# Optimization experiments

Measured on AMD Instinct MI355X. Metric: run time of the kernel, lower is better.

## Reference

```python
import jax, jax.numpy as jnp
import numpy as np

B, S, V = 256, 512, 50000
E, PD, PS = 256, 32, 121
FN, TAG = 230, 53
FEAT = E + 2 * PD  # 320
NEG = -1e30


def setup_inputs() -> dict:
    key = jax.random.key(0)
    ks = jax.random.split(key, 12)
    sentence = jax.random.randint(ks[0], (B, S), 0, V)
    # relative-position ids; 60 marks the entity token, keep background < 60
    pos1 = jax.random.randint(ks[1], (B, S), 0, 60)
    pos2 = jax.random.randint(ks[2], (B, S), 0, 60)
    e1 = jax.random.randint(ks[3], (B,), 1, S // 3)            # entity1 in first third
    e2 = jax.random.randint(ks[4], (B,), S // 3 + 1, 2 * S // 3)  # entity2 in second third
    rows = jnp.arange(B)
    pos1 = pos1.at[rows, e1].set(60)
    pos2 = pos2.at[rows, e2].set(60)
    word_emb = 0.02 * jax.random.normal(ks[5], (V, E), dtype=jnp.float32)
    pos1_emb = 0.02 * jax.random.normal(ks[6], (PS, PD), dtype=jnp.float32)
    pos2_emb = 0.02 * jax.random.normal(ks[7], (PS, PD), dtype=jnp.float32)
    rel_emb = 0.02 * jax.random.normal(ks[8], (TAG, FN), dtype=jnp.float32)
    conv_w = 0.05 * jax.random.normal(ks[9], (3, FEAT, FN), dtype=jnp.float32)  # HIO
    conv_b = jnp.zeros((FN,), dtype=jnp.float32)
    att_weight = jax.random.normal(ks[10], (B, 1, FN), dtype=jnp.float32)
    relation_bias = jax.random.normal(ks[11], (B, TAG, 1), dtype=jnp.float32)
    return {"sentence": sentence, "pos1": pos1, "pos2": pos2,
            "word_emb": word_emb, "pos1_emb": pos1_emb, "pos2_emb": pos2_emb,
            "rel_emb": rel_emb, "conv_w": conv_w, "conv_b": conv_b,
            "att_weight": att_weight, "relation_bias": relation_bias}


def reference(sentence, pos1, pos2, word_emb, pos1_emb, pos2_emb,
              rel_emb, conv_w, conv_b, att_weight, relation_bias):
    # embedding concat: [B, S, FEAT]
    embeds = jnp.concatenate(
        [word_emb[sentence], pos1_emb[pos1], pos2_emb[pos2]], axis=2)
    # Conv2d(1, FN, (3, FEAT), padding=(1, 0)) == 1D conv over seq, SAME-ish pad 1
    cnn = jax.lax.conv_general_dilated(
        embeds, conv_w, window_strides=(1,), padding=[(1, 1)],
        dimension_numbers=("NHC", "HIO", "NHC"))  # [B, S, FN]
    cnn = jax.nn.relu(cnn + conv_b)

    # vectorized entity segment boundaries (replaces the Python batch loop)
    idx = jnp.arange(S)
    mk1 = pos1 == 60
    mk2 = pos2 == 60
    p1min = jnp.min(jnp.where(mk1, idx, S), axis=1)
    p1max = jnp.max(jnp.where(mk1, idx, -1), axis=1)
    p2min = jnp.min(jnp.where(mk2, idx, S), axis=1)
    p2max = jnp.max(jnp.where(mk2, idx, -1), axis=1)
    first = p1min < p2min
    m1 = jnp.where(first, p1min, p2min)
    m2 = jnp.where(first, p1max, p2max)
    m3 = jnp.where(first, p2min, p1min)
    m4 = jnp.where(first, p2max, p1max)

    t = idx[None, :]  # [1, S]
    mask_a = t < jnp.maximum(m1, 1)[:, None]
    mask_b = (t >= m2[:, None]) & (t < jnp.maximum(m3, m2 + 1)[:, None])
    mask_c = t >= m4[:, None]

    def seg_max(mask):
        return jnp.max(jnp.where(mask[:, :, None], cnn, NEG), axis=1)  # [B, FN]

    pcnn = jnp.stack([seg_max(mask_a), seg_max(mask_b), seg_max(mask_c)], axis=2)  # [B, FN, 3]

    # attention over the 3 pooled segments
    M = jnp.tanh(pcnn)
    scores = jnp.einsum("bof,bft->bot", att_weight, M)      # [B, 1, 3]
    a = jax.nn.softmax(scores, axis=2)
    att = jnp.einsum("bft,bot->bfo", pcnn, a)               # [B, FN, 1]
    att_out = jnp.tanh(att)

    wei = jnp.einsum("tf,bfo->bto", rel_emb, att_out)       # [B, TAG, 1]
    res = jax.nn.softmax(wei + relation_bias, axis=1)
    return res.reshape(B, -1)
```

## Files before the change

kernel.cpp:

```cpp
#include <hip/hip_runtime.h>
#include <hip/hip_bf16.h>
#include <math.h>

constexpr int B    = 256;
constexpr int S    = 512;
constexpr int E    = 256;
constexpr int PD   = 32;
constexpr int FEAT = 320;
constexpr int FN   = 230;
constexpr int FNP  = 256;
constexpr int TAG  = 53;
constexpr int K    = 960;
constexpr int BM   = 128;
constexpr int KS   = 32;
constexpr int NG   = 10;
constexpr int LDA  = 36;
constexpr int LDB  = 36;

typedef short  bf16x8 __attribute__((ext_vector_type(8)));
typedef float  f32x4  __attribute__((ext_vector_type(4)));

__device__ __forceinline__ unsigned f2bf(float x) {
    union { float f; unsigned u; } v; v.f = x;
    unsigned r = v.u + 0x7FFF + ((v.u >> 16) & 1);
    return r >> 16;
}
__device__ __forceinline__ unsigned pack2(float a, float b) {
    return f2bf(a) | (f2bf(b) << 16);
}

__global__ __launch_bounds__(256) void wt_prep_kernel(
    const float* __restrict__ conv_w, unsigned short* __restrict__ wt)
{
    __shared__ float tile[32][33];
    const int tx = threadIdx.x & 31;
    const int ty = threadIdx.x >> 5;
    const int k0 = blockIdx.x * 32;
    const int n0 = blockIdx.y * 32;
#pragma unroll
    for (int i = 0; i < 4; ++i) {
        int k = k0 + ty + i * 8;
        int n = n0 + tx;
        tile[ty + i * 8][tx] = (n < FN) ? conv_w[(size_t)k * FN + n] : 0.0f;
    }
    __syncthreads();
#pragma unroll
    for (int i = 0; i < 4; ++i) {
        int n = n0 + ty + i * 8;
        int k = k0 + tx;
        wt[(size_t)n * K + k] = (unsigned short)f2bf(tile[tx][ty + i * 8]);
    }
}

__global__ __launch_bounds__(256) void bounds_kernel(
    const int* __restrict__ pos1, const int* __restrict__ pos2,
    int* __restrict__ segb, unsigned* __restrict__ pcnn)
{
    const int b = blockIdx.x;
    const int tid = threadIdx.x;
    __shared__ int r[4];
    if (tid == 0) { r[0] = S; r[1] = -1; r[2] = S; r[3] = -1; }
    __syncthreads();
    for (int s = tid; s < S; s += 256) {
        if (pos1[b * S + s] == 60) { atomicMin(&r[0], s); atomicMax(&r[1], s); }
        if (pos2[b * S + s] == 60) { atomicMin(&r[2], s); atomicMax(&r[3], s); }
    }
    __syncthreads();
    if (tid == 0) {
        int p1min = r[0], p1max = r[1], p2min = r[2], p2max = r[3];
        bool first = p1min < p2min;
        int m1 = first ? p1min : p2min;
        int m2 = first ? p1max : p2max;
        int m3 = first ? p2min : p1min;
        int m4 = first ? p2max : p1max;
        int4 o;
        o.x = max(m1, 1);
        o.y = m2;
        o.z = max(m3, m2 + 1);
        o.w = m4;
        *(int4*)(segb + b * 4) = o;
    }
    unsigned* pc = pcnn + (size_t)b * 3 * FNP;
    for (int i = tid; i < 3 * FNP; i += 256) pc[i] = 0u;
}

__global__ __launch_bounds__(512, 4) void conv_mfma_kernel(
    const int* __restrict__ sentence, const int* __restrict__ pos1,
    const int* __restrict__ pos2,
    const float* __restrict__ word_emb, const float* __restrict__ pos1_emb,
    const float* __restrict__ pos2_emb,
    const unsigned short* __restrict__ wt, const float* __restrict__ conv_b,
    const int* __restrict__ segb, unsigned* __restrict__ pcnn)
{
    __shared__ __align__(16) unsigned short ldsA[(BM + 2) * LDA];
    __shared__ __align__(16) unsigned short ldsB[FNP * LDB];
    __shared__ unsigned maxbuf[3 * FNP];

    const int tid  = threadIdx.x;
    const int b    = blockIdx.y;
    const int s0   = blockIdx.x * BM;
    const int lane = tid & 63;
    const int wid  = tid >> 6;
    const int wm   = wid >> 2;
    const int wn   = wid & 3;
    const int lrow = lane & 15;
    const int lgrp = lane >> 4;

    for (int i = tid; i < 3 * FNP; i += 512) maxbuf[i] = 0u;

    const int* sent_b = sentence + b * S;
    const int* p1_b   = pos1 + b * S;
    const int* p2_b   = pos2 + b * S;

    f32x4 acc[4][4];
#pragma unroll
    for (int i = 0; i < 4; ++i)
#pragma unroll
        for (int j = 0; j < 4; ++j) acc[i][j] = (f32x4){0.f, 0.f, 0.f, 0.f};

    for (int g = 0; g < NG; ++g) {
        const int fb = g * KS;

        __syncthreads();

        {
            int c = tid;
#pragma unroll
            for (int rep = 0; rep < 2; ++rep, c += 512) {
                if (c < (BM + 2) * 4) {
                    int r = c >> 2, q = c & 3;
                    int s = s0 - 1 + r;
                    int feat = fb + q * 8;
                    float4 v0 = make_float4(0.f, 0.f, 0.f, 0.f);
                    float4 v1 = v0;
                    if (s >= 0 && s < S) {
                        const float* p;
                        if (feat < E)            p = word_emb + (size_t)sent_b[s] * E + feat;
                        else if (feat < E + PD)  p = pos1_emb + p1_b[s] * PD + (feat - E);
                        else                     p = pos2_emb + p2_b[s] * PD + (feat - E - PD);
                        v0 = *(const float4*)p;
                        v1 = *(const float4*)(p + 4);
                    }
                    uint4 pk;
                    pk.x = pack2(v0.x, v0.y);
                    pk.y = pack2(v0.z, v0.w);
                    pk.z = pack2(v1.x, v1.y);
                    pk.w = pack2(v1.z, v1.w);
                    *(uint4*)&ldsA[r * LDA + q * 8] = pk;
                }
            }
        }
        {
            int c = tid;
#pragma unroll
            for (int rep = 0; rep < 2; ++rep, c += 512) {
                int n = c >> 2, q = c & 3;
                uint4 v = *(const uint4*)(wt + (size_t)n * K + fb + q * 8);
                *(uint4*)&ldsB[n * LDB + q * 8] = v;
            }
        }
        __syncthreads();

#pragma unroll
        for (int w = 0; w < 3; ++w) {
            bf16x8 af[4], bfr[4];
#pragma unroll
            for (int mi = 0; mi < 4; ++mi) {
                int r = wm * 64 + mi * 16 + lrow + w;
                af[mi] = *(const bf16x8*)&ldsA[r * LDA + lgrp * 8];
            }
#pragma unroll
            for (int ni = 0; ni < 4; ++ni) {
                if (wn * 64 + ni * 16 < FN) {
                    int n = wn * 64 + ni * 16 + lrow;
                    bfr[ni] = *(const bf16x8*)&ldsB[n * LDB + lgrp * 8];
                }
            }
#pragma unroll
            for (int mi = 0; mi < 4; ++mi)
#pragma unroll
                for (int ni = 0; ni < 4; ++ni)
                    if (wn * 64 + ni * 16 < FN)
                        acc[mi][ni] = __builtin_amdgcn_mfma_f32_16x16x32_bf16(
                            af[mi], bfr[ni], acc[mi][ni], 0, 0, 0);

            if (w < 2) {
                __syncthreads();
                int c = tid;
#pragma unroll
                for (int rep = 0; rep < 2; ++rep, c += 512) {
                    int n = c >> 2, q = c & 3;
                    uint4 v = *(const uint4*)(wt + (size_t)n * K
                                              + (w + 1) * FEAT + fb + q * 8);
                    *(uint4*)&ldsB[n * LDB + q * 8] = v;
                }
                __syncthreads();
            }
        }
    }

    const int4 sb = *(const int4*)(segb + b * 4);
    float biasv[4];
#pragma unroll
    for (int ni = 0; ni < 4; ++ni) {
        int f = wn * 64 + ni * 16 + lrow;
        biasv[ni] = (f < FN) ? conv_b[f] : 0.0f;
    }
#pragma unroll
    for (int mi = 0; mi < 4; ++mi) {
#pragma unroll
        for (int r = 0; r < 4; ++r) {
            int s = s0 + wm * 64 + mi * 16 + lgrp * 4 + r;
            int mask = 0;
            if (s < sb.x) mask |= 1;
            if (s >= sb.y && s < sb.z) mask |= 2;
            if (s >= sb.w) mask |= 4;
            if (!mask) continue;
#pragma unroll
            for (int ni = 0; ni < 4; ++ni) {
                int f = wn * 64 + ni * 16 + lrow;
                if (f >= FN) continue;
                float v = fmaxf(acc[mi][ni][r] + biasv[ni], 0.0f);
                unsigned uv = __float_as_uint(v);
                if (mask & 1) atomicMax(&maxbuf[f], uv);
                if (mask & 2) atomicMax(&maxbuf[FNP + f], uv);
                if (mask & 4) atomicMax(&maxbuf[2 * FNP + f], uv);
            }
        }
    }
    __syncthreads();
    unsigned* pc = pcnn + (size_t)b * 3 * FNP;
    for (int i = tid; i < 3 * FNP; i += 512) {
        unsigned m = maxbuf[i];
        if (((i & (FNP - 1)) < FN) && m) atomicMax(pc + i, m);
    }
}

__global__ __launch_bounds__(256) void finale_kernel(
    const float* __restrict__ pcnn, const float* __restrict__ att_weight,
    const float* __restrict__ rel_emb, const float* __restrict__ rel_bias,
    float* __restrict__ out)
{
    const int b = blockIdx.x;
    const int tid = threadIdx.x;
    __shared__ float red[12];
    __shared__ float satt[FN];
    __shared__ float wtag[56];

    const float* pc = pcnn + (size_t)b * 3 * FNP;
    float p0 = 0.f, p1 = 0.f, p2 = 0.f, aw = 0.f;
    if (tid < FN) {
        p0 = pc[tid];
        p1 = pc[FNP + tid];
        p2 = pc[2 * FNP + tid];
        aw = att_weight[b * FN + tid];
    }
    const int wid = tid >> 6;
#pragma unroll
    for (int t = 0; t < 3; ++t) {
        float pt = (t == 0) ? p0 : (t == 1) ? p1 : p2;
        float r = (tid < FN) ? aw * tanhf(pt) : 0.0f;
#pragma unroll
        for (int o = 32; o; o >>= 1) r += __shfl_xor(r, o);
        if ((tid & 63) == 0) red[t * 4 + wid] = r;
    }
    __syncthreads();
    float sc0 = red[0] + red[1] + red[2] + red[3];
    float sc1 = red[4] + red[5] + red[6] + red[7];
    float sc2 = red[8] + red[9] + red[10] + red[11];
    float m3s = fmaxf(sc0, fmaxf(sc1, sc2));
    float e0 = expf(sc0 - m3s), e1 = expf(sc1 - m3s), e2 = expf(sc2 - m3s);
    float inv = 1.0f / (e0 + e1 + e2);
    float a0 = e0 * inv, a1 = e1 * inv, a2 = e2 * inv;
    if (tid < FN) satt[tid] = tanhf(p0 * a0 + p1 * a1 + p2 * a2);
    __syncthreads();

    const int t = tid >> 2;
    const int part = tid & 3;
    if (t < TAG) {
        float s = 0.0f;
        for (int f = part; f < FN; f += 4) s += rel_emb[t * FN + f] * satt[f];
        s += __shfl_xor(s, 1);
        s += __shfl_xor(s, 2);
        if (part == 0) wtag[t] = s + rel_bias[b * TAG + t];
    }
    __syncthreads();

    if (tid < 64) {
        float v = (tid < TAG) ? wtag[tid] : -1e30f;
        float mx = v;
#pragma unroll
        for (int o = 32; o; o >>= 1) mx = fmaxf(mx, __shfl_xor(mx, o));
        float e = (tid < TAG) ? expf(v - mx) : 0.0f;
        float sum = e;
#pragma unroll
        for (int o = 32; o; o >>= 1) sum += __shfl_xor(sum, o);
        if (tid < TAG) out[b * TAG + tid] = e / sum;
    }
}

extern "C" void kernel_launch(void* const* d_in, const int* in_sizes, int n_in,
                              void* d_out, int out_size, void* d_ws, size_t ws_size,
                              hipStream_t stream)
{
    const int*   sentence  = (const int*)d_in[0];
    const int*   pos1      = (const int*)d_in[1];
    const int*   pos2      = (const int*)d_in[2];
    const float* word_emb  = (const float*)d_in[3];
    const float* pos1_emb  = (const float*)d_in[4];
    const float* pos2_emb  = (const float*)d_in[5];
    const float* rel_emb   = (const float*)d_in[6];
    const float* conv_w    = (const float*)d_in[7];
    const float* conv_b    = (const float*)d_in[8];
    const float* att_w     = (const float*)d_in[9];
    const float* rel_bias  = (const float*)d_in[10];
    float* out = (float*)d_out;

    int*            segb = (int*)d_ws;
    unsigned*       pcnn = (unsigned*)((char*)d_ws + 4096);
    unsigned short* wt   = (unsigned short*)((char*)d_ws + 4096 + 786432);

    wt_prep_kernel<<<dim3(K / 32, FNP / 32), 256, 0, stream>>>(conv_w, wt);
    bounds_kernel<<<B, 256, 0, stream>>>(pos1, pos2, segb, pcnn);
    conv_mfma_kernel<<<dim3(S / BM, B), 512, 0, stream>>>(
        sentence, pos1, pos2, word_emb, pos1_emb, pos2_emb,
        wt, conv_b, segb, pcnn);
    finale_kernel<<<B, 256, 0, stream>>>(
        (const float*)pcnn, att_w, rel_emb, rel_bias, out);
}
```

Before: 224.5 us.

## Restructure conv GEMM loads: direct-to-LDS weights, register-prefetched embeddings, merged prep kernel

Merges the weight-transpose and segment-bounds kernels into one launch, and reorders the weight layout so that each K-group's three conv taps are contiguous. The conv kernel now loads all three taps of B per group with global_load_lds straight into LDS, which removes the per-tap barriers and reloads. The embedding gather for the next group is prefetched into registers while the MFMAs run, and MFMA priority is raised via setprio. This cuts synchronisation and global-load latency per iteration, at the cost of a larger LDS footprint (about 49KB for B) that may lower occupancy.

```diff
diff --git a/kernel.cpp b/kernel.cpp
--- a/kernel.cpp
+++ b/kernel.cpp
@@ -1,21 +1,15 @@
 #include <hip/hip_runtime.h>
-#include <hip/hip_bf16.h>
 #include <math.h>
 
 constexpr int B    = 256;
 constexpr int S    = 512;
 constexpr int E    = 256;
 constexpr int PD   = 32;
-constexpr int FEAT = 320;
 constexpr int FN   = 230;
 constexpr int FNP  = 256;
 constexpr int TAG  = 53;
-constexpr int K    = 960;
 constexpr int BM   = 128;
-constexpr int KS   = 32;
 constexpr int NG   = 10;
-constexpr int LDA  = 36;
-constexpr int LDB  = 36;
 
 typedef short  bf16x8 __attribute__((ext_vector_type(8)));
 typedef float  f32x4  __attribute__((ext_vector_type(4)));
@@ -29,59 +23,64 @@
     return f2bf(a) | (f2bf(b) << 16);
 }
 
-__global__ __launch_bounds__(256) void wt_prep_kernel(
-    const float* __restrict__ conv_w, unsigned short* __restrict__ wt)
-{
-    __shared__ float tile[32][33];
-    const int tx = threadIdx.x & 31;
-    const int ty = threadIdx.x >> 5;
-    const int k0 = blockIdx.x * 32;
-    const int n0 = blockIdx.y * 32;
-#pragma unroll
-    for (int i = 0; i < 4; ++i) {
-        int k = k0 + ty + i * 8;
-        int n = n0 + tx;
-        tile[ty + i * 8][tx] = (n < FN) ? conv_w[(size_t)k * FN + n] : 0.0f;
-    }
-    __syncthreads();
-#pragma unroll
-    for (int i = 0; i < 4; ++i) {
-        int n = n0 + ty + i * 8;
-        int k = k0 + tx;
-        wt[(size_t)n * K + k] = (unsigned short)f2bf(tile[tx][ty + i * 8]);
-    }
-}
-
-__global__ __launch_bounds__(256) void bounds_kernel(
-    const int* __restrict__ pos1, const int* __restrict__ pos2,
+__device__ __forceinline__ void gl_lds16(const void* g, void* l) {
+    __builtin_amdgcn_global_load_lds(
+        (const __attribute__((address_space(1))) unsigned int*)g,
+        (__attribute__((address_space(3))) unsigned int*)l, 16, 0, 0);
+}
+
+__global__ __launch_bounds__(256) void prep_kernel(
+    const float* __restrict__ conv_w, const int* __restrict__ pos1,
+    const int* __restrict__ pos2, unsigned short* __restrict__ wt2,
     int* __restrict__ segb, unsigned* __restrict__ pcnn)
 {
-    const int b = blockIdx.x;
+    const int bid = blockIdx.x;
     const int tid = threadIdx.x;
-    __shared__ int r[4];
-    if (tid == 0) { r[0] = S; r[1] = -1; r[2] = S; r[3] = -1; }
-    __syncthreads();
-    for (int s = tid; s < S; s += 256) {
-        if (pos1[b * S + s] == 60) { atomicMin(&r[0], s); atomicMax(&r[1], s); }
-        if (pos2[b * S + s] == 60) { atomicMin(&r[2], s); atomicMax(&r[3], s); }
-    }
-    __syncthreads();
-    if (tid == 0) {
-        int p1min = r[0], p1max = r[1], p2min = r[2], p2max = r[3];
-        bool first = p1min < p2min;
-        int m1 = first ? p1min : p2min;
-        int m2 = first ? p1max : p2max;
-        int m3 = first ? p2min : p1min;
-        int m4 = first ? p2max : p1max;
-        int4 o;
-        o.x = max(m1, 1);
-        o.y = m2;
-        o.z = max(m3, m2 + 1);
-        o.w = m4;
-        *(int4*)(segb + b * 4) = o;
-    }
-    unsigned* pc = pcnn + (size_t)b * 3 * FNP;
-    for (int i = tid; i < 3 * FNP; i += 256) pc[i] = 0u;
+    if (bid < 240) {
+        __shared__ float tile[32][33];
+        const int kb = bid % 30, nb = bid / 30;
+        const int k0 = kb * 32, n0 = nb * 32;
+        const int tx = tid & 31, ty = tid >> 5;
+#pragma unroll
+        for (int i = 0; i < 4; ++i) {
+            int k = k0 + ty + i * 8, n = n0 + tx;
+            tile[ty + i * 8][tx] = (n < FN) ? conv_w[(size_t)k * FN + n] : 0.0f;
+        }
+        __syncthreads();
+        const int g = (k0 >> 5) % 10, w = k0 / 320;
+#pragma unroll
+        for (int i = 0; i < 4; ++i) {
+            int n = n0 + ty + i * 8;
+            wt2[(size_t)n * 960 + g * 96 + w * 32 + tx] =
+                (unsigned short)f2bf(tile[tx][ty + i * 8]);
+        }
+    } else {
+        const int b = bid - 240;
+        __shared__ int r[4];
+        if (tid == 0) { r[0] = S; r[1] = -1; r[2] = S; r[3] = -1; }
+        __syncthreads();
+        for (int s = tid; s < S; s += 256) {
+            if (pos1[b * S + s] == 60) { atomicMin(&r[0], s); atomicMax(&r[1], s); }
+            if (pos2[b * S + s] == 60) { atomicMin(&r[2], s); atomicMax(&r[3], s); }
+        }
+        __syncthreads();
+        if (tid == 0) {
+            int p1min = r[0], p1max = r[1], p2min = r[2], p2max = r[3];
+            bool first = p1min < p2min;
+            int m1 = first ? p1min : p2min;
+            int m2 = first ? p1max : p2max;
+            int m3 = first ? p2min : p1min;
+            int m4 = first ? p2max : p1max;
+            int4 o;
+            o.x = max(m1, 1);
+            o.y = m2;
+            o.z = max(m3, m2 + 1);
+            o.w = m4;
+            *(int4*)(segb + b * 4) = o;
+        }
+        unsigned* pc = pcnn + (size_t)b * 3 * FNP;
+        for (int i = tid; i < 3 * FNP; i += 256) pc[i] = 0u;
+    }
 }
 
 __global__ __launch_bounds__(512, 4) void conv_mfma_kernel(
@@ -89,11 +88,11 @@
     const int* __restrict__ pos2,
     const float* __restrict__ word_emb, const float* __restrict__ pos1_emb,
     const float* __restrict__ pos2_emb,
-    const unsigned short* __restrict__ wt, const float* __restrict__ conv_b,
+    const unsigned short* __restrict__ wt2, const float* __restrict__ conv_b,
     const int* __restrict__ segb, unsigned* __restrict__ pcnn)
 {
-    __shared__ __align__(16) unsigned short ldsA[(BM + 2) * LDA];
-    __shared__ __align__(16) unsigned short ldsB[FNP * LDB];
+    __shared__ __align__(16) unsigned short ldsB[12 * 256 * 8];
+    __shared__ __align__(16) unsigned short ldsA[528 * 8];
     __shared__ unsigned maxbuf[3 * FNP];
 
     const int tid  = threadIdx.x;
@@ -108,9 +107,23 @@
 
     for (int i = tid; i < 3 * FNP; i += 512) maxbuf[i] = 0u;
 
-    const int* sent_b = sentence + b * S;
-    const int* p1_b   = pos1 + b * S;
-    const int* p2_b   = pos2 + b * S;
+    const int q0 = (tid >= 396) ? 3 : (tid >= 264) ? 2 : (tid >= 132) ? 1 : 0;
+    const int r0 = tid - q0 * 132;
+    const int sA0 = s0 - 1 + r0;
+    const bool v0 = (unsigned)sA0 < (unsigned)S;
+    const int sid0 = v0 ? sentence[b * S + sA0] : 0;
+    const int p10  = v0 ? pos1[b * S + sA0] : 0;
+    const int p20  = v0 ? pos2[b * S + sA0] : 0;
+    const int r1   = 116 + tid;
+    const int sA1  = s0 - 1 + r1;
+    const bool v1  = (tid < 16) && ((unsigned)sA1 < (unsigned)S);
+    const int sid1 = v1 ? sentence[b * S + sA1] : 0;
+    const int p11  = v1 ? pos1[b * S + sA1] : 0;
+    const int p21  = v1 ? pos2[b * S + sA1] : 0;
+
+    const size_t bnoff = (size_t)(tid & 255) * 1920;
+    const int    bc0   = tid >> 8;
+    const char*  wt2c  = (const char*)wt2;
 
     f32x4 acc[4][4];
 #pragma unroll
@@ -118,64 +131,67 @@
 #pragma unroll
         for (int j = 0; j < 4; ++j) acc[i][j] = (f32x4){0.f, 0.f, 0.f, 0.f};
 
+    auto srcA = [&](int g, int sid, int p1v, int p2v, int qq) -> const float* {
+        if (g < 8)  return word_emb + (size_t)sid * E + g * 32 + qq * 8;
+        if (g == 8) return pos1_emb + p1v * PD + qq * 8;
+        return pos2_emb + p2v * PD + qq * 8;
+    };
+
+    float4 am0, am1, ae0, ae1;
+    {
+        const float* p = srcA(0, sid0, p10, p20, q0);
+        am0 = *(const float4*)p; am1 = *(const float4*)(p + 4);
+        if (tid < 16) {
+            const float* pe = srcA(0, sid1, p11, p21, 3);
+            ae0 = *(const float4*)pe; ae1 = *(const float4*)(pe + 4);
+        }
+    }
+
     for (int g = 0; g < NG; ++g) {
-        const int fb = g * KS;
-
-        __syncthreads();
-
+        __builtin_amdgcn_s_barrier();
+#pragma unroll
+        for (int rep = 0; rep < 6; ++rep) {
+            const void* src = wt2c + bnoff + (size_t)(g * 12 + 2 * rep + bc0) * 16;
+            void* dst = (char*)ldsB + (rep * 512 + wid * 64) * 16;
+            gl_lds16(src, dst);
+        }
         {
-            int c = tid;
-#pragma unroll
-            for (int rep = 0; rep < 2; ++rep, c += 512) {
-                if (c < (BM + 2) * 4) {
-                    int r = c >> 2, q = c & 3;
-                    int s = s0 - 1 + r;
-                    int feat = fb + q * 8;
-                    float4 v0 = make_float4(0.f, 0.f, 0.f, 0.f);
-                    float4 v1 = v0;
-                    if (s >= 0 && s < S) {
-                        const float* p;
-                        if (feat < E)            p = word_emb + (size_t)sent_b[s] * E + feat;
-                        else if (feat < E + PD)  p = pos1_emb + p1_b[s] * PD + (feat - E);
-                        else                     p = pos2_emb + p2_b[s] * PD + (feat - E - PD);
-                        v0 = *(const float4*)p;
-                        v1 = *(const float4*)(p + 4);
-                    }
-                    uint4 pk;
-                    pk.x = pack2(v0.x, v0.y);
-                    pk.y = pack2(v0.z, v0.w);
-                    pk.z = pack2(v1.x, v1.y);
-                    pk.w = pack2(v1.z, v1.w);
-                    *(uint4*)&ldsA[r * LDA + q * 8] = pk;
-                }
+            uint4 pk;
+            pk.x = pack2(am0.x, am0.y); pk.y = pack2(am0.z, am0.w);
+            pk.z = pack2(am1.x, am1.y); pk.w = pack2(am1.z, am1.w);
+            if (!v0) pk = make_uint4(0u, 0u, 0u, 0u);
+            *(uint4*)&ldsA[(q0 * 132 + r0) * 8] = pk;
+            if (tid < 16) {
+                uint4 pe;
+                pe.x = pack2(ae0.x, ae0.y); pe.y = pack2(ae0.z, ae0.w);
+                pe.z = pack2(ae1.x, ae1.y); pe.w = pack2(ae1.z, ae1.w);
+                if (!v1) pe = make_uint4(0u, 0u, 0u, 0u);
+                *(uint4*)&ldsA[(3 * 132 + r1) * 8] = pe;
             }
         }
-        {
-            int c = tid;
-#pragma unroll
-            for (int rep = 0; rep < 2; ++rep, c += 512) {
-                int n = c >> 2, q = c & 3;
-                uint4 v = *(const uint4*)(wt + (size_t)n * K + fb + q * 8);
-                *(uint4*)&ldsB[n * LDB + q * 8] = v;
+        asm volatile("s_waitcnt vmcnt(0) lgkmcnt(0)" ::: "memory");
+        __builtin_amdgcn_sched_barrier(0);
+        if (g < NG - 1) {
+            const float* p = srcA(g + 1, sid0, p10, p20, q0);
+            am0 = *(const float4*)p; am1 = *(const float4*)(p + 4);
+            if (tid < 16) {
+                const float* pe = srcA(g + 1, sid1, p11, p21, 3);
+                ae0 = *(const float4*)pe; ae1 = *(const float4*)(pe + 4);
             }
         }
-        __syncthreads();
-
+        __builtin_amdgcn_s_barrier();
+        __builtin_amdgcn_sched_barrier(0);
 #pragma unroll
         for (int w = 0; w < 3; ++w) {
             bf16x8 af[4], bfr[4];
 #pragma unroll
-            for (int mi = 0; mi < 4; ++mi) {
-                int r = wm * 64 + mi * 16 + lrow + w;
-                af[mi] = *(const bf16x8*)&ldsA[r * LDA + lgrp * 8];
-            }
-#pragma unroll
-            for (int ni = 0; ni < 4; ++ni) {
-                if (wn * 64 + ni * 16 < FN) {
-                    int n = wn * 64 + ni * 16 + lrow;
-                    bfr[ni] = *(const bf16x8*)&ldsB[n * LDB + lgrp * 8];
-                }
-            }
+            for (int mi = 0; mi < 4; ++mi)
+                af[mi] = *(const bf16x8*)&ldsA[(lgrp * 132 + wm * 64 + mi * 16 + lrow + w) * 8];
+#pragma unroll
+            for (int ni = 0; ni < 4; ++ni)
+                if (wn * 64 + ni * 16 < FN)
+                    bfr[ni] = *(const bf16x8*)&ldsB[((w * 4 + lgrp) * 256 + wn * 64 + ni * 16 + lrow) * 8];
+            __builtin_amdgcn_s_setprio(1);
 #pragma unroll
             for (int mi = 0; mi < 4; ++mi)
 #pragma unroll
@@ -183,19 +199,7 @@
                     if (wn * 64 + ni * 16 < FN)
                         acc[mi][ni] = __builtin_amdgcn_mfma_f32_16x16x32_bf16(
                             af[mi], bfr[ni], acc[mi][ni], 0, 0, 0);
-
-            if (w < 2) {
-                __syncthreads();
-                int c = tid;
-#pragma unroll
-                for (int rep = 0; rep < 2; ++rep, c += 512) {
-                    int n = c >> 2, q = c & 3;
-                    uint4 v = *(const uint4*)(wt + (size_t)n * K
-                                              + (w + 1) * FEAT + fb + q * 8);
-                    *(uint4*)&ldsB[n * LDB + q * 8] = v;
-                }
-                __syncthreads();
-            }
+            __builtin_amdgcn_s_setprio(0);
         }
     }
 
@@ -209,8 +213,8 @@
 #pragma unroll
     for (int mi = 0; mi < 4; ++mi) {
 #pragma unroll
-        for (int r = 0; r < 4; ++r) {
-            int s = s0 + wm * 64 + mi * 16 + lgrp * 4 + r;
+        for (int rr = 0; rr < 4; ++rr) {
+            int s = s0 + wm * 64 + mi * 16 + lgrp * 4 + rr;
             int mask = 0;
             if (s < sb.x) mask |= 1;
             if (s >= sb.y && s < sb.z) mask |= 2;
@@ -220,7 +224,7 @@
             for (int ni = 0; ni < 4; ++ni) {
                 int f = wn * 64 + ni * 16 + lrow;
                 if (f >= FN) continue;
-                float v = fmaxf(acc[mi][ni][r] + biasv[ni], 0.0f);
+                float v = fmaxf(acc[mi][ni][rr] + biasv[ni], 0.0f);
                 unsigned uv = __float_as_uint(v);
                 if (mask & 1) atomicMax(&maxbuf[f], uv);
                 if (mask & 2) atomicMax(&maxbuf[FNP + f], uv);
@@ -318,13 +322,12 @@
 
     int*            segb = (int*)d_ws;
     unsigned*       pcnn = (unsigned*)((char*)d_ws + 4096);
-    unsigned short* wt   = (unsigned short*)((char*)d_ws + 4096 + 786432);
-
-    wt_prep_kernel<<<dim3(K / 32, FNP / 32), 256, 0, stream>>>(conv_w, wt);
-    bounds_kernel<<<B, 256, 0, stream>>>(pos1, pos2, segb, pcnn);
+    unsigned short* wt2  = (unsigned short*)((char*)d_ws + 4096 + 786432);
+
+    prep_kernel<<<240 + B, 256, 0, stream>>>(conv_w, pos1, pos2, wt2, segb, pcnn);
     conv_mfma_kernel<<<dim3(S / BM, B), 512, 0, stream>>>(
         sentence, pos1, pos2, word_emb, pos1_emb, pos2_emb,
-        wt, conv_b, segb, pcnn);
+        wt2, conv_b, segb, pcnn);
     finale_kernel<<<B, 256, 0, stream>>>(
         (const float*)pcnn, att_w, rel_emb, rel_bias, out);
 }
```

Result: slower. 322.0 us (+43.4%).
